# Kernel tuning notes

Measured on AMD Instinct MI355X. Metric: run time of the kernel, lower is better.

Reference implementation:

```python
import jax, jax.numpy as jnp
import numpy as np

B, L, D, K, H = 2, 384, 1024, 128, 32
NUM_EDGES = 25600
NUM_T = 1000
SCALING = K ** -0.5
SQRT_2PI = float(np.sqrt(2.0 * np.pi))


def setup_inputs() -> dict:
    key = jax.random.key(0)
    ks = jax.random.split(key, 20)
    s = 0.02
    inp = {}
    inp["token_id"] = jax.random.randint(ks[0], (B, L), 0, 160)
    inp["is_periodic"] = jnp.zeros((B,), dtype=bool)
    inp["pos"] = 5.0 * jax.random.normal(ks[1], (B, L, 3), dtype=jnp.float32)
    inp["adj"] = jnp.ones((B, L, L), dtype=bool)
    inp["node_type_edge"] = jax.random.randint(ks[2], (B, L, L, 2), 0, NUM_EDGES)
    inp["time_step"] = jax.random.uniform(ks[3], (B, L), dtype=jnp.float32)
    inp["clean_mask"] = jnp.zeros((B, L), dtype=bool)
    # parameters
    inp["embed_w"] = s * jax.random.normal(ks[4], (160, D), dtype=jnp.float32)
    inp["Wpos"] = s * jax.random.normal(ks[5], (K, 3), dtype=jnp.float32)
    inp["Wpfe"] = s * jax.random.normal(ks[6], (D, K), dtype=jnp.float32)
    inp["gbf_means"] = jax.random.normal(ks[7], (K,), dtype=jnp.float32)
    inp["gbf_stds"] = 0.5 + jax.random.uniform(ks[8], (K,), dtype=jnp.float32)
    inp["gbf_mul"] = 1.0 + s * jax.random.normal(ks[9], (NUM_EDGES, 1), dtype=jnp.float32)
    inp["gbf_bias"] = s * jax.random.normal(ks[10], (NUM_EDGES, 1), dtype=jnp.float32)
    inp["W1"] = s * jax.random.normal(ks[11], (K, K), dtype=jnp.float32)
    inp["b1"] = jnp.zeros((K,), dtype=jnp.float32)
    inp["W2"] = s * jax.random.normal(ks[12], (H, K), dtype=jnp.float32)
    inp["b2"] = jnp.zeros((H,), dtype=jnp.float32)
    inp["Wproj"] = s * jax.random.normal(ks[13], (D, K), dtype=jnp.float32)
    inp["bproj"] = jnp.zeros((D,), dtype=jnp.float32)
    inp["Wt1"] = s * jax.random.normal(ks[14], (D, D), dtype=jnp.float32)
    inp["bt1"] = jnp.zeros((D,), dtype=jnp.float32)
    inp["Wt2"] = s * jax.random.normal(ks[15], (D, D), dtype=jnp.float32)
    inp["bt2"] = jnp.zeros((D,), dtype=jnp.float32)
    return inp


def _forward(token_id, is_periodic, pos, adj, node_type_edge, time_step, clean_mask,
             embed_w, Wpos, Wpfe, gbf_means, gbf_stds, gbf_mul, gbf_bias,
             W1, b1, W2, b2, Wproj, bproj, Wt1, bt1, Wt2, bt2):
    padding_mask = token_id == 0                                  # (B,L)
    molecule_mask = (token_id <= 129) & (~is_periodic[:, None])   # (B,L)
    x = embed_w[token_id]                                         # (B,L,D)

    # ---- _pos_emb (non-PBC branch: expand_pos = pos, expand_mask = padding_mask) ----
    delta = pos[:, :, None, :] - pos[:, None, :, :]               # (B,L,L,3)
    dist = jnp.sqrt(jnp.maximum(jnp.sum(delta * delta, -1), 1e-12))  # (B,L,L), safe norm

    # GaussianLayer
    mul = gbf_mul[node_type_edge].sum(-2)                         # (B,L,L,1)
    bias = gbf_bias[node_type_edge].sum(-2)                       # (B,L,L,1)
    y = mul * dist[..., None] + bias                              # (B,L,L,1) -> broadcast K
    std = jnp.abs(gbf_stds) + 1e-5
    a = (y - gbf_means) / std
    edge_feature = jnp.exp(-0.5 * a * a) / (SQRT_2PI * std)       # (B,L,L,K)

    # NonLinear projection to per-head bias
    gab = jax.nn.gelu(edge_feature @ W1.T + b1, approximate=False) @ W2.T + b2  # (B,L,L,H)
    gab = jnp.where(padding_mask[:, None, :, None], -jnp.inf, gab)  # expand-col mask
    gab = jnp.where(padding_mask[:, :, None, None], 0.0, gab)       # padding-row mask
    pos_attn_bias = jnp.transpose(gab, (0, 3, 1, 2))              # (B,H,L,L)

    d = gab.sum(-1)                                               # (B,L,L) sum over heads
    minv = jnp.finfo(jnp.float32).min
    d = jnp.where(padding_mask[:, None, :], minv, d)
    d = jnp.where(padding_mask[:, :, None], minv, d)
    adj_eff = adj | (~molecule_mask[:, :, None])
    d = jnp.where(~adj_eff, minv, d)
    attn = jax.nn.softmax(d * SCALING, axis=-1)                   # (B,L,L)

    pos_e = pos @ Wpos.T                                          # (B,L,K)
    pos_e = jnp.where(padding_mask[..., None], 0.0, pos_e)
    pfe = jnp.einsum('bij,bjk->bik', attn, pos_e)                 # (B,L,K)
    pfe = pfe @ Wpfe.T                                            # (B,L,D)

    ef = jnp.where(padding_mask[:, None, :, None], 0.0, edge_feature).sum(-2)  # (B,L,K)
    pfe = pfe + ef @ Wproj.T + bproj
    pos_embedding = jnp.where(padding_mask[..., None], 0.0, pfe)  # (B,L,D)

    # ---- time step encoder (sinusoidal + MLP) ----
    t = jnp.where(clean_mask, 0.0, time_step) * NUM_T             # (B,L)
    half = D // 2
    freqs = jnp.exp(-jnp.log(10000.0) * jnp.arange(half, dtype=jnp.float32) / half)
    ang = t[..., None] * freqs                                    # (B,L,half)
    sin_emb = jnp.concatenate([jnp.sin(ang), jnp.cos(ang)], -1)   # (B,L,D)
    time_embed = jax.nn.silu(sin_emb @ Wt1.T + bt1) @ Wt2.T + bt2

    x = x + time_embed + pos_embedding
    return x, padding_mask, time_embed, pos_attn_bias, pos_embedding


def reference(token_id, is_periodic, pos, adj, node_type_edge, time_step, clean_mask,
              embed_w, Wpos, Wpfe, gbf_means, gbf_stds, gbf_mul, gbf_bias,
              W1, b1, W2, b2, Wproj, bproj, Wt1, bt1, Wt2, bt2):
    return _forward(token_id, is_periodic, pos, adj, node_type_edge, time_step, clean_mask,
                    embed_w, Wpos, Wpfe, gbf_means, gbf_stds, gbf_mul, gbf_bias,
                    W1, b1, W2, b2, Wproj, bproj, Wt1, bt1, Wt2, bt2)
```

## Files before the change

### kernel.cpp

```cpp
#include <hip/hip_runtime.h>
#include <stddef.h>

#define B_ 2
#define L_ 384
#define D_ 1024
#define K_ 128
#define H_ 32

#define MINV (-3.402823466e38f)
#define NEG_BIG (-1.0e38f)
#define SCALING_ 0.08838834764831845f
#define INV_SQRT_2PI 0.3989422804014327f

typedef __attribute__((ext_vector_type(8))) short bf16x8;
typedef __attribute__((ext_vector_type(4))) float f32x4;

__device__ __forceinline__ float finitize(float x) {
    return fminf(fmaxf(x, -1.0e38f), 1.0e38f);
}
__device__ __forceinline__ unsigned short f2bf(float x) {
    unsigned int u = __float_as_uint(x);
    u += 0x7FFFu + ((u >> 16) & 1u);
    return (unsigned short)(u >> 16);
}
__device__ __forceinline__ unsigned short f2bf_rtz(float x) {
    return (unsigned short)(__float_as_uint(x) >> 16);
}
__device__ __forceinline__ float gelu_tanh(float x) {
    const float x2 = x * x;
    const float z = x * fmaf(0.0356774081f, x2, 0.7978845608f);
    const float e = __expf(2.0f * z);
    const float t = fmaf(-2.0f, __builtin_amdgcn_rcpf(e + 1.0f), 1.0f);
    const float hx = 0.5f * x;
    return fmaf(hx, t, hx);
}

__global__ __launch_bounds__(256) void prep_sin_kernel(
    const float* __restrict__ W1, const float* __restrict__ W2,
    const float* __restrict__ Wpfe, const float* __restrict__ Wproj,
    const float* __restrict__ Wt2,
    unsigned short* __restrict__ W1bf, unsigned short* __restrict__ W2bf,
    unsigned short* __restrict__ Wpfebf, unsigned short* __restrict__ Wprojbf,
    unsigned short* __restrict__ Wt2bf,
    const float* __restrict__ time_step, const unsigned char* __restrict__ clean,
    const int* __restrict__ token, unsigned short* __restrict__ sin_bf,
    float* __restrict__ padout)
{
    const int blk = blockIdx.x;
    if (blk < 1300) {
        const int i = blk * 256 + threadIdx.x;
        const float* src; unsigned short* dst; int off;
        if (i < 4096)       { src = W1;    dst = W1bf;    off = i; }
        else if (i < 5120)  { src = W2;    dst = W2bf;    off = i - 4096; }
        else if (i < 37888) { src = Wpfe;  dst = Wpfebf;  off = i - 5120; }
        else if (i < 70656) { src = Wproj; dst = Wprojbf; off = i - 37888; }
        else                { src = Wt2;   dst = Wt2bf;   off = i - 70656; }
        const float4 v = ((const float4*)src)[off];
        ushort4 p; p.x = f2bf(v.x); p.y = f2bf(v.y); p.z = f2bf(v.z); p.w = f2bf(v.w);
        ((ushort4*)dst)[off] = p;
    } else {
        const int row = blk - 1300;
        if (threadIdx.x == 0) padout[row] = (token[row] == 0) ? 1.0f : 0.0f;
        const float t = (clean[row] ? 0.0f : time_step[row]) * 1000.0f;
        for (int k = threadIdx.x; k < 512; k += 256) {
            const float f = __expf(-9.210340371976184f * (float)k * (1.0f / 512.0f));
            const float ang = t * f;
            sin_bf[(size_t)row * D_ + k]       = f2bf(__sinf(ang));
            sin_bf[(size_t)row * D_ + 512 + k] = f2bf(__cosf(ang));
        }
    }
}

__device__ __forceinline__ void gemm_ts_body(
    char* smem, int m0, int n0,
    const unsigned short* __restrict__ A, const float* __restrict__ Bw,
    const float* __restrict__ bias, void* __restrict__ Cv,
    int N, int Kd, int act)
{
    unsigned short (*sA)[72] = (unsigned short(*)[72])smem;
    unsigned short (*sB)[72] = (unsigned short(*)[72])(smem + 4608);
    const int tid  = threadIdx.x;
    const int lane = tid & 63;
    const int wave = tid >> 6;
    const int l15  = lane & 15;
    const int quad = lane >> 4;
    const int mt   = wave & 1;
    const int np   = wave >> 1;

    const int ar = tid >> 3, ac = (tid & 7) * 8;
    const int bc4 = (tid & 15) * 4;

    f32x4 acc[2];
#pragma unroll
    for (int t = 0; t < 2; ++t) acc[t] = (f32x4){0.f, 0.f, 0.f, 0.f};

    uint4 ra = *(const uint4*)&A[(size_t)(m0 + ar) * Kd + ac];
    float4 rbv[4];
#pragma unroll
    for (int c = 0; c < 4; ++c)
        rbv[c] = *(const float4*)&Bw[(size_t)(n0 + ((tid + c * 256) >> 4)) * Kd + bc4];

    for (int k0 = 0; k0 < Kd; k0 += 64) {
        *(uint4*)&sA[ar][ac] = ra;
#pragma unroll
        for (int c = 0; c < 4; ++c) {
            ushort4 p;
            p.x = f2bf(rbv[c].x); p.y = f2bf(rbv[c].y);
            p.z = f2bf(rbv[c].z); p.w = f2bf(rbv[c].w);
            *(ushort4*)&sB[(tid + c * 256) >> 4][bc4] = p;
        }
        __syncthreads();
        if (k0 + 64 < Kd) {
            ra = *(const uint4*)&A[(size_t)(m0 + ar) * Kd + k0 + 64 + ac];
#pragma unroll
            for (int c = 0; c < 4; ++c)
                rbv[c] = *(const float4*)&Bw[(size_t)(n0 + ((tid + c * 256) >> 4)) * Kd + k0 + 64 + bc4];
        }
#pragma unroll
        for (int kk = 0; kk < 64; kk += 32) {
            const bf16x8 av = *(const bf16x8*)&sA[mt * 16 + l15][kk + quad * 8];
#pragma unroll
            for (int t = 0; t < 2; ++t) {
                const bf16x8 bv = *(const bf16x8*)&sB[(np * 2 + t) * 16 + l15][kk + quad * 8];
                acc[t] = __builtin_amdgcn_mfma_f32_16x16x32_bf16(av, bv, acc[t], 0, 0, 0);
            }
        }
        __syncthreads();
    }
#pragma unroll
    for (int t = 0; t < 2; ++t) {
        const int nc = n0 + (np * 2 + t) * 16 + l15;
        const float bv = bias[nc];
#pragma unroll
        for (int r = 0; r < 4; ++r) {
            const int mr = m0 + mt * 16 + quad * 4 + r;
            float v = acc[t][r] + bv;
            if (act) {
                v = v / (1.0f + __expf(-v));
                ((unsigned short*)Cv)[(size_t)mr * N + nc] = f2bf(v);
            } else {
                ((float*)Cv)[(size_t)mr * N + nc] = v;
            }
        }
    }
}

__device__ __forceinline__ void edge_body(
    char* smem, int row,
    const int* __restrict__ token_id,
    const unsigned char* __restrict__ is_periodic,
    const float* __restrict__ pos,
    const unsigned char* __restrict__ adj,
    const int* __restrict__ nte,
    const float* __restrict__ gbf_means,
    const float* __restrict__ gbf_stds,
    const float* __restrict__ gbf_mul,
    const float* __restrict__ gbf_bias,
    const float* __restrict__ b1,
    const float* __restrict__ b2,
    const float* __restrict__ Wpos,
    const unsigned short* __restrict__ W1bf,
    const unsigned short* __restrict__ W2bf,
    unsigned short* __restrict__ pfe_bf,
    unsigned short* __restrict__ ef_bf,
    float* __restrict__ out_pab)
{
    const int b = row / L_;
    const int i = row - b * L_;
    const int tid = threadIdx.x;

    const int tok_i = token_id[row];
    if (tok_i == 0) {
        for (int idx = tid; idx < H_ * L_; idx += 256) {
            const int h = idx / L_;
            const int j = idx - h * L_;
            out_pab[((size_t)(b * H_ + h) * L_ + i) * L_ + j] = 0.0f;
        }
        if (tid < K_) {
            pfe_bf[(size_t)row * K_ + tid] = 0;
            ef_bf[(size_t)row * K_ + tid]  = 0;
        }
        return;
    }

    typedef unsigned short efbuf_t[32][136];
    efbuf_t* sEF = (efbuf_t*)smem;
    unsigned short (*sACT)[136] = (unsigned short(*)[136])(smem + 17408);
    float (*sGab)[33] = (float(*)[33])(smem + 26112);
    float* sD      = (float*)(smem + 30336);
    float* sRed    = (float*)(smem + 31872);
    float* sYall   = (float*)(smem + 32896);
    unsigned char* sPadCol = (unsigned char*)(smem + 34432);

    for (int j = tid; j < L_; j += 256)
        sPadCol[j] = (token_id[b * L_ + j] == 0) ? 1 : 0;

    const float px = pos[(size_t)row * 3 + 0];
    const float py = pos[(size_t)row * 3 + 1];
    const float pz = pos[(size_t)row * 3 + 2];
    for (int jg2 = tid; jg2 < L_; jg2 += 256) {
        const float dx = px - pos[(size_t)(b * L_ + jg2) * 3 + 0];
        const float dy = py - pos[(size_t)(b * L_ + jg2) * 3 + 1];
        const float dz = pz - pos[(size_t)(b * L_ + jg2) * 3 + 2];
        const float dist = sqrtf(fmaxf(dx * dx + dy * dy + dz * dz, 1e-12f));
        const size_t eoff = ((size_t)(b * L_ + i) * L_ + jg2) * 2;
        const int e0 = nte[eoff], e1 = nte[eoff + 1];
        sYall[jg2] = (gbf_mul[e0] + gbf_mul[e1]) * dist + (gbf_bias[e0] + gbf_bias[e1]);
    }

    const int lane = tid & 63;
    const int wave = tid >> 6;
    const int l15  = lane & 15;
    const int quad = lane >> 4;
    const int mt   = wave & 1;
    const int ntb  = (wave >> 1) * 4;
    float rb1[4];
#pragma unroll
    for (int nt = 0; nt < 4; ++nt) rb1[nt] = b1[(ntb + nt) * 16 + l15];
    const int hc = (wave >> 1) * 16 + l15;
    const float rb2 = b2[hc];
    bf16x8 w1f[4][4];
#pragma unroll
    for (int ks = 0; ks < 4; ++ks)
#pragma unroll
        for (int nt = 0; nt < 4; ++nt)
            w1f[ks][nt] = *(const bf16x8*)&W1bf[((ntb + nt) * 16 + l15) * K_ + ks * 32 + quad * 8];
    bf16x8 bv2[4];
#pragma unroll
    for (int ks = 0; ks < 4; ++ks)
        bv2[ks] = *(const bf16x8*)&W2bf[hc * K_ + ks * 32 + quad * 8];

    const int kg4 = (tid & 31) * 4;
    const int jg  = tid >> 5;
    const int jb  = jg * 4;
    float meanv[4], istdv[4], cKv[4];
#pragma unroll
    for (int c = 0; c < 4; ++c) {
        meanv[c] = gbf_means[kg4 + c];
        const float s = fabsf(gbf_stds[kg4 + c]) + 1e-5f;
        istdv[c] = 1.0f / s;
        cKv[c]   = INV_SQRT_2PI * istdv[c];
    }
    float efs[4] = {0.f, 0.f, 0.f, 0.f};

    __syncthreads();

#pragma unroll
    for (int jj = 0; jj < 4; ++jj) {
        const int j = jb + jj;
        const float y = sYall[j];
        const bool ok = !sPadCol[j];
        ushort4 p;
#pragma unroll
        for (int c = 0; c < 4; ++c) {
            const float a = (y - meanv[c]) * istdv[c];
            const float ef = __expf(-0.5f * a * a) * cKv[c];
            ((unsigned short*)&p)[c] = f2bf_rtz(ef);
            if (ok) efs[c] += ef;
        }
        *(ushort4*)&sEF[0][j][kg4] = p;
    }
    __syncthreads();

    for (int tile = 0; tile < L_ / 32; ++tile) {
        const int jt0 = tile * 32;
        const int cur = tile & 1, nxt = cur ^ 1;

        f32x4 acc1[4];
#pragma unroll
        for (int nt = 0; nt < 4; ++nt) acc1[nt] = (f32x4){0.f, 0.f, 0.f, 0.f};
#pragma unroll
        for (int ks = 0; ks < 4; ++ks) {
            const bf16x8 av = *(const bf16x8*)&sEF[cur][mt * 16 + l15][ks * 32 + quad * 8];
#pragma unroll
            for (int nt = 0; nt < 4; ++nt)
                acc1[nt] = __builtin_amdgcn_mfma_f32_16x16x32_bf16(av, w1f[ks][nt], acc1[nt], 0, 0, 0);
        }

        if (tile + 1 < L_ / 32) {
            const int jn0 = jt0 + 32;
#pragma unroll
            for (int jj = 0; jj < 4; ++jj) {
                const int j = jb + jj;
                const float y = sYall[jn0 + j];
                const bool ok = !sPadCol[jn0 + j];
                ushort4 p;
#pragma unroll
                for (int c = 0; c < 4; ++c) {
                    const float a = (y - meanv[c]) * istdv[c];
                    const float ef = __expf(-0.5f * a * a) * cKv[c];
                    ((unsigned short*)&p)[c] = f2bf_rtz(ef);
                    if (ok) efs[c] += ef;
                }
                *(ushort4*)&sEF[nxt][j][kg4] = p;
            }
        }

#pragma unroll
        for (int nt = 0; nt < 4; ++nt) {
            const int kkc = (ntb + nt) * 16 + l15;
#pragma unroll
            for (int r = 0; r < 4; ++r) {
                const float v = gelu_tanh(acc1[nt][r] + rb1[nt]);
                sACT[mt * 16 + quad * 4 + r][kkc] = f2bf_rtz(v);
            }
        }
        __syncthreads();

        f32x4 acc2 = (f32x4){0.f, 0.f, 0.f, 0.f};
#pragma unroll
        for (int ks = 0; ks < 4; ++ks) {
            const bf16x8 av = *(const bf16x8*)&sACT[mt * 16 + l15][ks * 32 + quad * 8];
            acc2 = __builtin_amdgcn_mfma_f32_16x16x32_bf16(av, bv2[ks], acc2, 0, 0, 0);
        }
        const int jl0 = mt * 16 + quad * 4;
#pragma unroll
        for (int r = 0; r < 4; ++r) sGab[jl0 + r][hc] = acc2[r] + rb2;
        __syncthreads();

        {
            const int h = tid >> 3, f = tid & 7;
            const int jb2 = f * 4;
            float4 st;
#pragma unroll
            for (int r = 0; r < 4; ++r) {
                float v = finitize(sGab[jb2 + r][h]);
                if (sPadCol[jt0 + jb2 + r]) v = NEG_BIG;
                ((float*)&st)[r] = v;
            }
            *(float4*)&out_pab[((size_t)(b * H_ + h) * L_ + i) * L_ + jt0 + jb2] = st;
        }
        if (tid < 32) {
            float s = 0.0f;
#pragma unroll
            for (int h = 0; h < 32; ++h) s += sGab[tid][h];
            sD[jt0 + tid] = s;
        }
    }

    {
        float* efScr = (float*)sACT;
#pragma unroll
        for (int c = 0; c < 4; ++c) efScr[jg * 128 + kg4 + c] = efs[c];
    }
    __syncthreads();
    if (tid < 128) {
        const float* efScr = (const float*)sACT;
        float s = 0.0f;
#pragma unroll
        for (int g = 0; g < 8; ++g) s += efScr[g * 128 + tid];
        ef_bf[(size_t)row * K_ + tid] = f2bf(s);
    }
    __syncthreads();

    const bool molecule = (tok_i <= 129) && (is_periodic[b] == 0);
    float lmax = -INFINITY;
    for (int j = tid; j < L_; j += 256) {
        const bool colpad = sPadCol[j] != 0;
        const bool adj_eff = (adj[((size_t)(b * L_ + i)) * L_ + j] != 0) || (!molecule);
        const float dv = (colpad || !adj_eff) ? MINV : sD[j];
        const float s = dv * SCALING_;
        sD[j] = s;
        lmax = fmaxf(lmax, s);
    }
#pragma unroll
    for (int off = 32; off > 0; off >>= 1) lmax = fmaxf(lmax, __shfl_xor(lmax, off));
    if (lane == 0) sRed[wave] = lmax;
    __syncthreads();
    const float smax = fmaxf(fmaxf(sRed[0], sRed[1]), fmaxf(sRed[2], sRed[3]));
    float lsum = 0.0f;
    for (int j = tid; j < L_; j += 256) {
        const float e = __expf(sD[j] - smax);
        sD[j] = e;
        lsum += e;
    }
#pragma unroll
    for (int off = 32; off > 0; off >>= 1) lsum += __shfl_xor(lsum, off);
    if (lane == 0) sRed[4 + wave] = lsum;
    __syncthreads();
    const float inv = 1.0f / (sRed[4] + sRed[5] + sRed[6] + sRed[7]);

    float a0 = 0.f, a1 = 0.f, a2 = 0.f;
    for (int j = tid; j < L_; j += 256) {
        if (!sPadCol[j]) {
            const float e = sD[j];
            a0 += e * pos[(size_t)(b * L_ + j) * 3 + 0];
            a1 += e * pos[(size_t)(b * L_ + j) * 3 + 1];
            a2 += e * pos[(size_t)(b * L_ + j) * 3 + 2];
        }
    }
#pragma unroll
    for (int off = 32; off > 0; off >>= 1) {
        a0 += __shfl_xor(a0, off);
        a1 += __shfl_xor(a1, off);
        a2 += __shfl_xor(a2, off);
    }
    if (lane == 0) { sRed[8 + wave] = a0; sRed[12 + wave] = a1; sRed[16 + wave] = a2; }
    __syncthreads();
    if (tid < 128) {
        const float m0 = sRed[8] + sRed[9] + sRed[10] + sRed[11];
        const float m1 = sRed[12] + sRed[13] + sRed[14] + sRed[15];
        const float m2 = sRed[16] + sRed[17] + sRed[18] + sRed[19];
        const float w0 = Wpos[tid * 3 + 0], w1 = Wpos[tid * 3 + 1], w2 = Wpos[tid * 3 + 2];
        pfe_bf[(size_t)row * K_ + tid] = f2bf((m0 * w0 + m1 * w1 + m2 * w2) * inv);
    }
}

__global__ __launch_bounds__(256, 3) void edge_ts1(
    const int* __restrict__ token_id,
    const unsigned char* __restrict__ is_periodic,
    const float* __restrict__ pos,
    const unsigned char* __restrict__ adj,
    const int* __restrict__ nte,
    const float* __restrict__ gbf_means,
    const float* __restrict__ gbf_stds,
    const float* __restrict__ gbf_mul,
    const float* __restrict__ gbf_bias,
    const float* __restrict__ b1,
    const float* __restrict__ b2,
    const float* __restrict__ Wpos,
    const unsigned short* __restrict__ W1bf,
    const unsigned short* __restrict__ W2bf,
    unsigned short* __restrict__ pfe_bf,
    unsigned short* __restrict__ ef_bf,
    float* __restrict__ out_pab,
    const unsigned short* __restrict__ sin_bf,
    const float* __restrict__ Wt1,
    const float* __restrict__ bt1,
    unsigned short* __restrict__ h1_bf)
{
    __shared__ __align__(16) char smem[34816];
    const int bx = blockIdx.x;
    if (bx < B_ * L_) {
        edge_body(smem, bx, token_id, is_periodic, pos, adj, nte,
                  gbf_means, gbf_stds, gbf_mul, gbf_bias, b1, b2, Wpos,
                  W1bf, W2bf, pfe_bf, ef_bf, out_pab);
    } else {
        const int tsb = bx - B_ * L_;
        const int m0 = (tsb >> 4) * 32;
        const int n0 = (tsb & 15) * 64;
        gemm_ts_body(smem, m0, n0, sin_bf, Wt1, bt1, (void*)h1_bf, D_, D_, 1);
    }
}

__global__ __launch_bounds__(256) void ts2_pe_kernel(
    const unsigned short* __restrict__ h1_bf,
    const unsigned short* __restrict__ Wt2bf,
    const float* __restrict__ bt2,
    const unsigned short* __restrict__ pfe_bf,
    const unsigned short* __restrict__ ef_bf,
    const unsigned short* __restrict__ Wpfebf,
    const unsigned short* __restrict__ Wprojbf,
    const float* __restrict__ bproj,
    const int* __restrict__ token,
    const float* __restrict__ embed_w,
    float* __restrict__ outTE,
    float* __restrict__ outPE,
    float* __restrict__ outX)
{
    __shared__ __align__(16) char smem[26112];
    const int tid  = threadIdx.x;
    const int lane = tid & 63;
    const int wave = tid >> 6;
    const int l15  = lane & 15;
    const int quad = lane >> 4;
    const int mt   = wave & 1;
    const int np   = wave >> 1;
    const int m0 = blockIdx.y * 32, n0 = blockIdx.x * 64;

    f32x4 accTE[2];
#pragma unroll
    for (int t = 0; t < 2; ++t) accTE[t] = (f32x4){0.f, 0.f, 0.f, 0.f};
    {
        unsigned short (*sA)[72] = (unsigned short(*)[72])smem;
        unsigned short (*sB)[72] = (unsigned short(*)[72])(smem + 4608);
        const int ar = tid >> 3, ac = (tid & 7) * 8;
        const int br1r = (tid + 256) >> 3;

        uint4 ra  = *(const uint4*)&h1_bf[(size_t)(m0 + ar) * D_ + ac];
        uint4 rb0 = *(const uint4*)&Wt2bf[(size_t)(n0 + ar) * D_ + ac];
        uint4 rb1 = *(const uint4*)&Wt2bf[(size_t)(n0 + br1r) * D_ + ac];

        for (int k0 = 0; k0 < D_; k0 += 64) {
            *(uint4*)&sA[ar][ac]   = ra;
            *(uint4*)&sB[ar][ac]   = rb0;
            *(uint4*)&sB[br1r][ac] = rb1;
            __syncthreads();
            if (k0 + 64 < D_) {
                ra  = *(const uint4*)&h1_bf[(size_t)(m0 + ar) * D_ + k0 + 64 + ac];
                rb0 = *(const uint4*)&Wt2bf[(size_t)(n0 + ar) * D_ + k0 + 64 + ac];
                rb1 = *(const uint4*)&Wt2bf[(size_t)(n0 + br1r) * D_ + k0 + 64 + ac];
            }
#pragma unroll
            for (int kk = 0; kk < 64; kk += 32) {
                const bf16x8 av = *(const bf16x8*)&sA[mt * 16 + l15][kk + quad * 8];
#pragma unroll
                for (int t = 0; t < 2; ++t) {
                    const bf16x8 bv = *(const bf16x8*)&sB[(np * 2 + t) * 16 + l15][kk + quad * 8];
                    accTE[t] = __builtin_amdgcn_mfma_f32_16x16x32_bf16(av, bv, accTE[t], 0, 0, 0);
                }
            }
            __syncthreads();
        }
    }

    unsigned short (*sA2)[136] = (unsigned short(*)[136])smem;
    unsigned short (*sB2)[136] = (unsigned short(*)[136])(smem + 8704);
    f32x4 accPE[2];
#pragma unroll
    for (int t = 0; t < 2; ++t) accPE[t] = (f32x4){0.f, 0.f, 0.f, 0.f};

    for (int phase = 0; phase < 2; ++phase) {
        const unsigned short* Ap = phase ? ef_bf : pfe_bf;
        const unsigned short* Bp = phase ? Wprojbf : Wpfebf;
#pragma unroll
        for (int e = tid; e < 512; e += 256) {
            const int r = e >> 4, c8 = (e & 15) * 8;
            *(uint4*)&sA2[r][c8] = *(const uint4*)&Ap[(size_t)(m0 + r) * K_ + c8];
        }
#pragma unroll
        for (int e = tid; e < 1024; e += 256) {
            const int r = e >> 4, c8 = (e & 15) * 8;
            *(uint4*)&sB2[r][c8] = *(const uint4*)&Bp[(size_t)(n0 + r) * K_ + c8];
        }
        __syncthreads();
#pragma unroll
        for (int ks = 0; ks < 4; ++ks) {
            const bf16x8 av = *(const bf16x8*)&sA2[mt * 16 + l15][ks * 32 + quad * 8];
#pragma unroll
            for (int t = 0; t < 2; ++t) {
                const bf16x8 bv = *(const bf16x8*)&sB2[(np * 2 + t) * 16 + l15][ks * 32 + quad * 8];
                accPE[t] = __builtin_amdgcn_mfma_f32_16x16x32_bf16(av, bv, accPE[t], 0, 0, 0);
            }
        }
        __syncthreads();
    }

#pragma unroll
    for (int t = 0; t < 2; ++t) {
        const int nc = n0 + (np * 2 + t) * 16 + l15;
        const float bte = bt2[nc];
        const float bpe = bproj[nc];
#pragma unroll
        for (int r = 0; r < 4; ++r) {
            const int mr = m0 + mt * 16 + quad * 4 + r;
            const int tok = token[mr];
            const float te = accTE[t][r] + bte;
            const float pe = (tok == 0) ? 0.0f : (accPE[t][r] + bpe);
            outTE[(size_t)mr * D_ + nc] = te;
            outPE[(size_t)mr * D_ + nc] = pe;
            outX[(size_t)mr * D_ + nc] = embed_w[(size_t)tok * D_ + nc] + te + pe;
        }
    }
}

extern "C" void kernel_launch(void* const* d_in, const int* in_sizes, int n_in,
                              void* d_out, int out_size, void* d_ws, size_t ws_size,
                              hipStream_t stream) {
    const int*           token_id    = (const int*)d_in[0];
    const unsigned char* is_periodic = (const unsigned char*)d_in[1];
    const float*         pos         = (const float*)d_in[2];
    const unsigned char* adj         = (const unsigned char*)d_in[3];
    const int*           nte         = (const int*)d_in[4];
    const float*         time_step   = (const float*)d_in[5];
    const unsigned char* clean_mask  = (const unsigned char*)d_in[6];
    const float*         embed_w     = (const float*)d_in[7];
    const float*         Wpos        = (const float*)d_in[8];
    const float*         Wpfe        = (const float*)d_in[9];
    const float*         gbf_means   = (const float*)d_in[10];
    const float*         gbf_stds    = (const float*)d_in[11];
    const float*         gbf_mul     = (const float*)d_in[12];
    const float*         gbf_bias    = (const float*)d_in[13];
    const float*         W1          = (const float*)d_in[14];
    const float*         b1          = (const float*)d_in[15];
    const float*         W2          = (const float*)d_in[16];
    const float*         b2          = (const float*)d_in[17];
    const float*         Wproj       = (const float*)d_in[18];
    const float*         bproj       = (const float*)d_in[19];
    const float*         Wt1         = (const float*)d_in[20];
    const float*         bt1         = (const float*)d_in[21];
    const float*         Wt2         = (const float*)d_in[22];
    const float*         bt2         = (const float*)d_in[23];

    float* out = (float*)d_out;
    float* out_x   = out;
    float* out_pad = out + 786432;
    float* out_te  = out + 787200;
    float* out_pab = out + 1573632;
    float* out_pe  = out + 11010816;

    unsigned short* wsu = (unsigned short*)d_ws;
    unsigned short* W1bf    = wsu;
    unsigned short* W2bf    = wsu + 16384;
    unsigned short* Wpfebf  = wsu + 20480;
    unsigned short* Wprojbf = wsu + 151552;
    unsigned short* Wt2bf   = wsu + 282624;
    unsigned short* sin_bf  = wsu + 1331200;
    unsigned short* h1_bf   = wsu + 2117632;
    unsigned short* pfe_bf  = wsu + 2904064;
    unsigned short* ef_bf   = wsu + 3002368;

    prep_sin_kernel<<<dim3(2068), dim3(256), 0, stream>>>(
        W1, W2, Wpfe, Wproj, Wt2, W1bf, W2bf, Wpfebf, Wprojbf, Wt2bf,
        time_step, clean_mask, token_id, sin_bf, out_pad);
    edge_ts1<<<dim3(B_ * L_ + 384), dim3(256), 0, stream>>>(
        token_id, is_periodic, pos, adj, nte, gbf_means, gbf_stds, gbf_mul, gbf_bias,
        b1, b2, Wpos, W1bf, W2bf, pfe_bf, ef_bf, out_pab,
        sin_bf, Wt1, bt1, h1_bf);
    ts2_pe_kernel<<<dim3(16, 24), dim3(256), 0, stream>>>(
        h1_bf, Wt2bf, bt2, pfe_bf, ef_bf, Wpfebf, Wprojbf, bproj, token_id, embed_w,
        out_te, out_pe, out_x);
}
```

Baseline: 181.9 us.

## Double-buffer activations, drop sGab staging, use exp2-based gelu and gaussian

The edge kernel now double-buffers the activation tile, which removes the second per-tile __syncthreads. Each wave writes its MFMA output for the attention bias straight to global memory, and the per-column head sums are done with shuffle reductions into two partial arrays instead of staging through a shared sGab buffer. The Gaussian basis is rewritten as a quadratic in y fed to a native exp2, and gelu_tanh is replaced by an equivalent exp2/rcp form with fewer ops. Shared memory grows to about 40KB and launch bounds ask for 4 blocks per CU, which may pressure registers. The global stores of pab become 16-byte segments per lane rather than the previous layout.

```diff
diff --git a/kernel.cpp b/kernel.cpp
--- a/kernel.cpp
+++ b/kernel.cpp
@@ -15,6 +15,9 @@
 typedef __attribute__((ext_vector_type(8))) short bf16x8;
 typedef __attribute__((ext_vector_type(4))) float f32x4;
 
+__device__ __forceinline__ float fast_exp2(float x) {
+    return __builtin_amdgcn_exp2f(x);
+}
 __device__ __forceinline__ float finitize(float x) {
     return fminf(fmaxf(x, -1.0e38f), 1.0e38f);
 }
@@ -26,13 +29,10 @@
 __device__ __forceinline__ unsigned short f2bf_rtz(float x) {
     return (unsigned short)(__float_as_uint(x) >> 16);
 }
-__device__ __forceinline__ float gelu_tanh(float x) {
-    const float x2 = x * x;
-    const float z = x * fmaf(0.0356774081f, x2, 0.7978845608f);
-    const float e = __expf(2.0f * z);
-    const float t = fmaf(-2.0f, __builtin_amdgcn_rcpf(e + 1.0f), 1.0f);
-    const float hx = 0.5f * x;
-    return fmaf(hx, t, hx);
+__device__ __forceinline__ float gelu_fast(float x) {
+    const float z2 = x * fmaf(0.10294324f, x * x, 2.3022083f);
+    const float e = fast_exp2(z2);
+    return fmaf(-x, __builtin_amdgcn_rcpf(e + 1.0f), x);
 }
 
 __global__ __launch_bounds__(256) void prep_sin_kernel(
@@ -184,13 +184,12 @@
     }
 
     typedef unsigned short efbuf_t[32][136];
-    efbuf_t* sEF = (efbuf_t*)smem;
-    unsigned short (*sACT)[136] = (unsigned short(*)[136])(smem + 17408);
-    float (*sGab)[33] = (float(*)[33])(smem + 26112);
-    float* sD      = (float*)(smem + 30336);
-    float* sRed    = (float*)(smem + 31872);
-    float* sYall   = (float*)(smem + 32896);
-    unsigned char* sPadCol = (unsigned char*)(smem + 34432);
+    efbuf_t* sEF  = (efbuf_t*)smem;
+    efbuf_t* sACT = (efbuf_t*)(smem + 17408);
+    float* sDp    = (float*)(smem + 34816);
+    float* sRed   = (float*)(smem + 37888);
+    float* sYall  = (float*)(smem + 38400);
+    unsigned char* sPadCol = (unsigned char*)(smem + 39936);
 
     for (int j = tid; j < L_; j += 256)
         sPadCol[j] = (token_id[b * L_ + j] == 0) ? 1 : 0;
@@ -213,11 +212,12 @@
     const int l15  = lane & 15;
     const int quad = lane >> 4;
     const int mt   = wave & 1;
-    const int ntb  = (wave >> 1) * 4;
+    const int np   = wave >> 1;
+    const int ntb  = np * 4;
     float rb1[4];
 #pragma unroll
     for (int nt = 0; nt < 4; ++nt) rb1[nt] = b1[(ntb + nt) * 16 + l15];
-    const int hc = (wave >> 1) * 16 + l15;
+    const int hc = np * 16 + l15;
     const float rb2 = b2[hc];
     bf16x8 w1f[4][4];
 #pragma unroll
@@ -233,13 +233,17 @@
     const int kg4 = (tid & 31) * 4;
     const int jg  = tid >> 5;
     const int jb  = jg * 4;
-    float meanv[4], istdv[4], cKv[4];
+    float A2v[4], A1v[4], A0v[4], cKv[4];
 #pragma unroll
     for (int c = 0; c < 4; ++c) {
-        meanv[c] = gbf_means[kg4 + c];
+        const float m = gbf_means[kg4 + c];
         const float s = fabsf(gbf_stds[kg4 + c]) + 1e-5f;
-        istdv[c] = 1.0f / s;
-        cKv[c]   = INV_SQRT_2PI * istdv[c];
+        const float istd = 1.0f / s;
+        const float c2 = -0.72134752f * istd * istd;
+        A2v[c] = c2;
+        A1v[c] = -2.0f * c2 * m;
+        A0v[c] = c2 * m * m;
+        cKv[c] = INV_SQRT_2PI * istd;
     }
     float efs[4] = {0.f, 0.f, 0.f, 0.f};
 
@@ -249,12 +253,13 @@
     for (int jj = 0; jj < 4; ++jj) {
         const int j = jb + jj;
         const float y = sYall[j];
+        const float y2 = y * y;
         const bool ok = !sPadCol[j];
         ushort4 p;
 #pragma unroll
         for (int c = 0; c < 4; ++c) {
-            const float a = (y - meanv[c]) * istdv[c];
-            const float ef = __expf(-0.5f * a * a) * cKv[c];
+            const float q = fmaf(A2v[c], y2, fmaf(A1v[c], y, A0v[c]));
+            const float ef = fast_exp2(q) * cKv[c];
             ((unsigned short*)&p)[c] = f2bf_rtz(ef);
             if (ok) efs[c] += ef;
         }
@@ -283,12 +288,13 @@
             for (int jj = 0; jj < 4; ++jj) {
                 const int j = jb + jj;
                 const float y = sYall[jn0 + j];
+                const float y2 = y * y;
                 const bool ok = !sPadCol[jn0 + j];
                 ushort4 p;
 #pragma unroll
                 for (int c = 0; c < 4; ++c) {
-                    const float a = (y - meanv[c]) * istdv[c];
-                    const float ef = __expf(-0.5f * a * a) * cKv[c];
+                    const float q = fmaf(A2v[c], y2, fmaf(A1v[c], y, A0v[c]));
+                    const float ef = fast_exp2(q) * cKv[c];
                     ((unsigned short*)&p)[c] = f2bf_rtz(ef);
                     if (ok) efs[c] += ef;
                 }
@@ -301,8 +307,8 @@
             const int kkc = (ntb + nt) * 16 + l15;
 #pragma unroll
             for (int r = 0; r < 4; ++r) {
-                const float v = gelu_tanh(acc1[nt][r] + rb1[nt]);
-                sACT[mt * 16 + quad * 4 + r][kkc] = f2bf_rtz(v);
+                const float v = gelu_fast(acc1[nt][r] + rb1[nt]);
+                sACT[cur][mt * 16 + quad * 4 + r][kkc] = f2bf_rtz(v);
             }
         }
         __syncthreads();
@@ -310,31 +316,33 @@
         f32x4 acc2 = (f32x4){0.f, 0.f, 0.f, 0.f};
 #pragma unroll
         for (int ks = 0; ks < 4; ++ks) {
-            const bf16x8 av = *(const bf16x8*)&sACT[mt * 16 + l15][ks * 32 + quad * 8];
+            const bf16x8 av = *(const bf16x8*)&sACT[cur][mt * 16 + l15][ks * 32 + quad * 8];
             acc2 = __builtin_amdgcn_mfma_f32_16x16x32_bf16(av, bv2[ks], acc2, 0, 0, 0);
         }
-        const int jl0 = mt * 16 + quad * 4;
-#pragma unroll
-        for (int r = 0; r < 4; ++r) sGab[jl0 + r][hc] = acc2[r] + rb2;
-        __syncthreads();
-
-        {
-            const int h = tid >> 3, f = tid & 7;
-            const int jb2 = f * 4;
-            float4 st;
-#pragma unroll
-            for (int r = 0; r < 4; ++r) {
-                float v = finitize(sGab[jb2 + r][h]);
-                if (sPadCol[jt0 + jb2 + r]) v = NEG_BIG;
-                ((float*)&st)[r] = v;
-            }
-            *(float4*)&out_pab[((size_t)(b * H_ + h) * L_ + i) * L_ + jt0 + jb2] = st;
-        }
-        if (tid < 32) {
-            float s = 0.0f;
-#pragma unroll
-            for (int h = 0; h < 32; ++h) s += sGab[tid][h];
-            sD[jt0 + tid] = s;
+
+        const int jcol = jt0 + mt * 16 + quad * 4;
+        const uchar4 pc = *(const uchar4*)&sPadCol[jcol];
+        float4 st;
+        float dvv[4];
+#pragma unroll
+        for (int r = 0; r < 4; ++r) {
+            const float v = acc2[r] + rb2;
+            dvv[r] = v;
+            float w = finitize(v);
+            if (((const unsigned char*)&pc)[r]) w = NEG_BIG;
+            ((float*)&st)[r] = w;
+        }
+        *(float4*)&out_pab[((size_t)(b * H_ + hc) * L_ + i) * L_ + jcol] = st;
+
+#pragma unroll
+        for (int off = 1; off < 16; off <<= 1) {
+#pragma unroll
+            for (int r = 0; r < 4; ++r) dvv[r] += __shfl_xor(dvv[r], off);
+        }
+        if (l15 == 0) {
+            float4 dq;
+            dq.x = dvv[0]; dq.y = dvv[1]; dq.z = dvv[2]; dq.w = dvv[3];
+            *(float4*)&sDp[np * 384 + jcol] = dq;
         }
     }
 
@@ -358,9 +366,10 @@
     for (int j = tid; j < L_; j += 256) {
         const bool colpad = sPadCol[j] != 0;
         const bool adj_eff = (adj[((size_t)(b * L_ + i)) * L_ + j] != 0) || (!molecule);
-        const float dv = (colpad || !adj_eff) ? MINV : sD[j];
+        const float dval = sDp[j] + sDp[384 + j];
+        const float dv = (colpad || !adj_eff) ? MINV : dval;
         const float s = dv * SCALING_;
-        sD[j] = s;
+        sDp[j] = s;
         lmax = fmaxf(lmax, s);
     }
 #pragma unroll
@@ -370,8 +379,8 @@
     const float smax = fmaxf(fmaxf(sRed[0], sRed[1]), fmaxf(sRed[2], sRed[3]));
     float lsum = 0.0f;
     for (int j = tid; j < L_; j += 256) {
-        const float e = __expf(sD[j] - smax);
-        sD[j] = e;
+        const float e = __expf(sDp[j] - smax);
+        sDp[j] = e;
         lsum += e;
     }
 #pragma unroll
@@ -383,7 +392,7 @@
     float a0 = 0.f, a1 = 0.f, a2 = 0.f;
     for (int j = tid; j < L_; j += 256) {
         if (!sPadCol[j]) {
-            const float e = sD[j];
+            const float e = sDp[j];
             a0 += e * pos[(size_t)(b * L_ + j) * 3 + 0];
             a1 += e * pos[(size_t)(b * L_ + j) * 3 + 1];
             a2 += e * pos[(size_t)(b * L_ + j) * 3 + 2];
@@ -406,7 +415,7 @@
     }
 }
 
-__global__ __launch_bounds__(256, 3) void edge_ts1(
+__global__ __launch_bounds__(256, 4) void edge_ts1(
     const int* __restrict__ token_id,
     const unsigned char* __restrict__ is_periodic,
     const float* __restrict__ pos,
@@ -429,7 +438,7 @@
     const float* __restrict__ bt1,
     unsigned short* __restrict__ h1_bf)
 {
-    __shared__ __align__(16) char smem[34816];
+    __shared__ __align__(16) char smem[40320];
     const int bx = blockIdx.x;
     if (bx < B_ * L_) {
         edge_body(smem, bx, token_id, is_periodic, pos, adj, nte,
```

Measured after the change: 227.7 us. 1.25x slower.
